# Performance work log

Hardware: AMD Instinct MI355X
Metric: run time of the kernel (lower is better)

Reference implementation:

```python
import jax, jax.numpy as jnp
import numpy as np

TOPK = 8            # args.topk
SWAP_RATIO = 0.3    # args.swap_ratio
NUM_SPECIAL = 999   # first non-special wordpiece id in bert-base-uncased


def setup_inputs() -> dict:
    key = jax.random.key(0)
    k0, k1, k2, k3, k4, k5 = jax.random.split(key, 6)
    B, S, V, D = 4, 512, 30522, 768
    return {
        "delta_grad": jax.random.normal(k0, (B, S, D), jnp.float32),
        "src_embeds": jax.random.normal(k1, (B, S, D), jnp.float32),
        "embedding_matrix": jax.random.normal(k2, (V, D), jnp.float32),
        "src_tokens": jax.random.randint(k3, (B, S), 0, V),
        "pred_lm": jax.random.normal(k4, (B, S, V), jnp.float32),
        "attention_mask": jnp.ones((B, S), jnp.int32),
        "rand_u": jax.random.uniform(k5, (B, S), jnp.float32),
    }


def reference(delta_grad, src_embeds, embedding_matrix, src_tokens, pred_lm, attention_mask, rand_u):
    B, S, D = delta_grad.shape
    V = embedding_matrix.shape[0]
    neg_inf = jnp.float32(-np.inf)

    # dir_dot_grad = -(prev_dot - new_dot) = new_dot - prev_dot
    new_dot = jnp.einsum('bsd,vd->bsv', delta_grad, embedding_matrix)   # [B,S,V]
    prev_dot = jnp.einsum('bsd,bsd->bs', delta_grad, src_embeds)        # [B,S]
    dir_dot_grad = new_dot - prev_dot[..., None]

    # pairwise euclidean distance between src_embeds and vocab embeddings
    src_sq = jnp.sum(src_embeds * src_embeds, axis=-1)                  # [B,S]
    vocab_sq = jnp.sum(embedding_matrix * embedding_matrix, axis=-1)    # [V]
    dot = jnp.einsum('bsd,vd->bsv', src_embeds, embedding_matrix)       # [B,S,V]
    sq_norm = src_sq[..., None] + vocab_sq[None, None, :] - 2.0 * dot
    dir_norm = jnp.sqrt(jax.nn.relu(sq_norm) + 1e-20)

    dir_dot_grad = dir_dot_grad / dir_norm

    # LM top-k allowed-token mask (scatter of 0 into a -inf mask in torch)
    _, topk_idx = jax.lax.top_k(pred_lm, TOPK)                          # [B,S,K]
    topk_idx = topk_idx * attention_mask[..., None].astype(topk_idx.dtype)
    bi = jnp.arange(B)[:, None, None]
    si = jnp.arange(S)[None, :, None]
    allowed = jnp.zeros((B, S, V), bool).at[bi, si, topk_idx].set(True)

    filtered = jnp.where(allowed, dir_dot_grad, neg_inf)
    # special tokens [:999] -> -inf (overrides any topk scatter there)
    filtered = jnp.where(jnp.arange(V)[None, None, :] < NUM_SPECIAL, neg_inf, filtered)
    # forbid keeping the original token
    filtered = jnp.where(jnp.arange(V)[None, None, :] == src_tokens[..., None], neg_inf, filtered)

    adv_flip = jnp.argmax(filtered, axis=2)                             # [B,S]

    # swap mask: non-special positions, Bernoulli(swap_ratio)
    no_special = src_tokens >= NUM_SPECIAL
    swap = rand_u > (1.0 - SWAP_RATIO)
    mask_idx = (no_special & swap).astype(src_tokens.dtype)

    adv_tokens = src_tokens * (1 - mask_idx) + adv_flip.astype(src_tokens.dtype) * mask_idx
    return adv_tokens
```

## Files before the change

kernel.cpp:

```cpp
#include <hip/hip_runtime.h>
#include <math.h>

constexpr int TOPK = 8;
constexpr int NUM_SPECIAL = 999;
constexpr int V = 30522;
constexpr int D = 768;
constexpr int BLOCK = 256;
constexpr int V2 = V / 2;
constexpr int NQ = 14;
constexpr int NK = (V2 + BLOCK - 1) / BLOCK;
constexpr int CAP = 512;
constexpr int HOTCAP = 64;

__device__ __forceinline__ unsigned long long fkey(float v, unsigned int idx) {
    unsigned int u = __float_as_uint(v);
    u = ((int)u < 0) ? ~u : (u | 0x80000000u);
    return ((unsigned long long)u << 32) | (unsigned long long)(~idx);
}

__device__ __forceinline__ void net8(float (&L)[TOPK], float t) {
    #pragma unroll
    for (int j = 0; j < TOPK; ++j) {
        float m = fmaxf(L[j], t); t = fminf(L[j], t); L[j] = m;
    }
}

__device__ __forceinline__ void cmpx(float& a, float& b) {
    float m = fmaxf(a, b), n = fminf(a, b); a = m; b = n;
}
__device__ __forceinline__ void bitonic_sort8_desc(float (&v)[TOPK]) {
    cmpx(v[0], v[4]); cmpx(v[1], v[5]); cmpx(v[2], v[6]); cmpx(v[3], v[7]);
    cmpx(v[0], v[2]); cmpx(v[1], v[3]); cmpx(v[4], v[6]); cmpx(v[5], v[7]);
    cmpx(v[0], v[1]); cmpx(v[2], v[3]); cmpx(v[4], v[5]); cmpx(v[6], v[7]);
}

__device__ __forceinline__ void wave_extract8(float (&cur)[TOPK], int lane,
                                              float* dst) {
    #pragma unroll
    for (int r = 0; r < TOPK; ++r) {
        float m = cur[0];
        int ml = lane;
        #pragma unroll
        for (int off = 1; off < 64; off <<= 1) {
            float om = __shfl_xor(m, off, 64);
            int   ol = __shfl_xor(ml, off, 64);
            if (om > m || (om == m && ol < ml)) { m = om; ml = ol; }
        }
        if (lane == ml) {
            #pragma unroll
            for (int j = 0; j < TOPK - 1; ++j) cur[j] = cur[j + 1];
            cur[TOPK - 1] = -INFINITY;
        }
        if (lane == 0) dst[r] = m;
    }
}

__global__ __launch_bounds__(BLOCK, 8) void dvat_kernel(
    const float* __restrict__ delta_grad,
    const float* __restrict__ src_embeds,
    const float* __restrict__ emb,
    const int*   __restrict__ src_tokens,
    const float* __restrict__ pred_lm,
    const int*   __restrict__ attn,
    const float* __restrict__ rand_u,
    int* __restrict__ out)
{
    const int pos = blockIdx.x;
    const int tid = threadIdx.x;
    const int lane = tid & 63;
    const int wave = tid >> 6;

    __shared__ float  sm32[32];
    __shared__ float  s_g8;
    __shared__ int    s_hot[HOTCAP];
    __shared__ int    s_nhot;
    __shared__ int    s_ncand;
    __shared__ unsigned long long sh_cand64[CAP];
    __shared__ int    s_cand[TOPK];
    __shared__ double s_scores[TOPK];
    __shared__ double s_pd[4], s_ssq[4];
    __shared__ float  shf[2 * D];

    if (tid == 0) { s_nhot = 0; s_ncand = 0; }

    const float2* row2 = (const float2*)(pred_lm + (size_t)pos * V);

    float vx[TOPK], vy[TOPK];
    #pragma unroll
    for (int j = 0; j < TOPK; ++j) { vx[j] = -INFINITY; vy[j] = -INFINITY; }

    int i = tid;
    for (int q = 0; q < NQ; ++q, i += 4 * BLOCK) {
        float2 a = row2[i];
        float2 b = row2[i + BLOCK];
        float2 c = row2[i + 2 * BLOCK];
        float2 d = row2[i + 3 * BLOCK];
        net8(vx, a.x); net8(vy, a.y);
        net8(vx, b.x); net8(vy, b.y);
        net8(vx, c.x); net8(vy, c.y);
        net8(vx, d.x); net8(vy, d.y);
    }
    for (; i < V2; i += BLOCK) {
        float2 f = row2[i];
        net8(vx, f.x); net8(vy, f.y);
    }

    float v8[TOPK];
    #pragma unroll
    for (int j = 0; j < TOPK; ++j) v8[j] = fmaxf(vx[j], vy[TOPK - 1 - j]);
    bitonic_sort8_desc(v8);
    const float tmax = v8[0];

    wave_extract8(v8, lane, &sm32[wave * 8]);
    __syncthreads();

    if (wave == 0) {
        float c = (lane < 32) ? sm32[lane] : -INFINITY;
        float m = -INFINITY;
        #pragma unroll
        for (int r = 0; r < TOPK; ++r) {
            m = c; int ml = lane;
            #pragma unroll
            for (int off = 1; off < 64; off <<= 1) {
                float om = __shfl_xor(m, off, 64);
                int   ol = __shfl_xor(ml, off, 64);
                if (om > m || (om == m && ol < ml)) { m = om; ml = ol; }
            }
            if (lane == ml) c = -INFINITY;
        }
        if (lane == 0) s_g8 = m;
    }
    __syncthreads();
    const float g8 = s_g8;

    if (tmax >= g8) {
        int p = atomicAdd(&s_nhot, 1);
        if (p < HOTCAP) s_hot[p] = tid;
    }
    __syncthreads();

    if (s_nhot <= HOTCAP) {
        const int nhot = s_nhot;
        const int total = nhot * NK;
        for (int w = tid; w < total; w += BLOCK) {
            const int h = w / NK;
            const int k = w - h * NK;
            const int i2 = s_hot[h] + (k << 8);
            if (i2 < V2) {
                float2 f = row2[i2];
                if (f.x >= g8) {
                    int p = atomicAdd(&s_ncand, 1);
                    if (p < CAP) sh_cand64[p] = fkey(f.x, (unsigned)(2 * i2));
                }
                if (f.y >= g8) {
                    int p = atomicAdd(&s_ncand, 1);
                    if (p < CAP) sh_cand64[p] = fkey(f.y, (unsigned)(2 * i2 + 1));
                }
            }
        }
    } else {
        for (int i2 = tid; i2 < V2; i2 += BLOCK) {
            float2 f = row2[i2];
            if (f.x >= g8) {
                int p = atomicAdd(&s_ncand, 1);
                if (p < CAP) sh_cand64[p] = fkey(f.x, (unsigned)(2 * i2));
            }
            if (f.y >= g8) {
                int p = atomicAdd(&s_ncand, 1);
                if (p < CAP) sh_cand64[p] = fkey(f.y, (unsigned)(2 * i2 + 1));
            }
        }
    }
    __syncthreads();
    const int ncand = min(s_ncand, CAP);

    for (int it = 0; it < TOPK; ++it) {
        if (tid < 64) {
            unsigned long long m = 0ull; int ms = 0;
            for (int j = tid; j < ncand; j += 64) {
                unsigned long long x = sh_cand64[j];
                if (x > m) { m = x; ms = j; }
            }
            #pragma unroll
            for (int off = 32; off; off >>= 1) {
                unsigned long long om = __shfl_down(m, off, 64);
                int os = __shfl_down(ms, off, 64);
                if (om > m) { m = om; ms = os; }
            }
            if (tid == 0) {
                s_cand[it] = (m == 0ull) ? 0 : (int)(~(unsigned int)m);
                sh_cand64[ms] = 0ull;
            }
        }
        __syncthreads();
    }

    if (tid == 0 && attn[pos] == 0) {
        #pragma unroll
        for (int k = 0; k < TOPK; ++k) s_cand[k] = 0;
    }
    __syncthreads();

    const float* dg = delta_grad + (size_t)pos * D;
    const float* se = src_embeds + (size_t)pos * D;

    double pd = 0.0, ssq = 0.0;
    for (int ii = tid; ii < D; ii += BLOCK) {
        float g = dg[ii], e = se[ii];
        shf[ii] = g;
        shf[D + ii] = e;
        pd  += (double)g * (double)e;
        ssq += (double)e * (double)e;
    }
    #pragma unroll
    for (int off = 32; off; off >>= 1) {
        pd  += __shfl_down(pd, off, 64);
        ssq += __shfl_down(ssq, off, 64);
    }
    if (lane == 0) { s_pd[wave] = pd; s_ssq[wave] = ssq; }
    __syncthreads();

    const double prev_dot = s_pd[0] + s_pd[1] + s_pd[2] + s_pd[3];
    const double src_sq   = s_ssq[0] + s_ssq[1] + s_ssq[2] + s_ssq[3];

    #pragma unroll
    for (int kk = 0; kk < 2; ++kk) {
        const int k = 2 * wave + kk;
        const int v = s_cand[k];
        const float* ev = emb + (size_t)v * D;
        double ddg = 0.0, dse = 0.0, dvv = 0.0;
        for (int ii = lane; ii < D; ii += 64) {
            double e = (double)ev[ii];
            ddg += e * (double)shf[ii];
            dse += e * (double)shf[D + ii];
            dvv += e * e;
        }
        #pragma unroll
        for (int off = 32; off; off >>= 1) {
            ddg += __shfl_down(ddg, off, 64);
            dse += __shfl_down(dse, off, 64);
            dvv += __shfl_down(dvv, off, 64);
        }
        if (lane == 0) {
            double sq = src_sq + dvv - 2.0 * dse;
            if (sq < 0.0) sq = 0.0;
            double dn = sqrt(sq + 1e-20);
            s_scores[k] = (ddg - prev_dot) / dn;
        }
    }
    __syncthreads();

    if (tid == 0) {
        const int src_tok = src_tokens[pos];
        int best = 0;
        double best_s = 0.0;
        bool found = false;
        #pragma unroll
        for (int k = 0; k < TOPK; ++k) {
            const int v = s_cand[k];
            if (v < NUM_SPECIAL || v == src_tok) continue;
            const double sc = s_scores[k];
            if (!found || sc > best_s || (sc == best_s && v < best)) {
                best = v; best_s = sc; found = true;
            }
        }
        const int adv_flip = found ? best : 0;
        const bool no_special = (src_tok >= NUM_SPECIAL);
        const bool swap = (rand_u[pos] > 0.7f);
        out[pos] = (no_special && swap) ? adv_flip : src_tok;
    }
}

extern "C" void kernel_launch(void* const* d_in, const int* in_sizes, int n_in,
                              void* d_out, int out_size, void* d_ws, size_t ws_size,
                              hipStream_t stream) {
    const float* delta_grad = (const float*)d_in[0];
    const float* src_embeds = (const float*)d_in[1];
    const float* emb        = (const float*)d_in[2];
    const int*   src_tokens = (const int*)d_in[3];
    const float* pred_lm    = (const float*)d_in[4];
    const int*   attn       = (const int*)d_in[5];
    const float* randu      = (const float*)d_in[6];
    int* out = (int*)d_out;

    const int BS = in_sizes[3];
    dvat_kernel<<<BS, BLOCK, 0, stream>>>(delta_grad, src_embeds, emb,
                                          src_tokens, pred_lm, attn, randu, out);
}
```

Baseline: 425.0 us.

## Replace per-thread top-8 network with per-thread max plus float4 row scans

The first pass over each pred_lm row now keeps only a running maximum per thread instead of an 8-wide insertion network, and derives the 8th-largest threshold from the 256 thread maxima. Rows are read as float4 with a parity-dependent 2-element offset for alignment, and the two leftover elements are checked separately by thread 0. The dot-product stage also uses float4 loads. This cuts ALU work in the memory-bound scan, but the looser threshold may admit more candidates and hot threads in the second pass.

Measured after the change: 414.5 us. 2.5% less time.

```diff
diff --git a/kernel.cpp b/kernel.cpp
--- a/kernel.cpp
+++ b/kernel.cpp
@@ -6,9 +6,8 @@
 constexpr int V = 30522;
 constexpr int D = 768;
 constexpr int BLOCK = 256;
-constexpr int V2 = V / 2;
-constexpr int NQ = 14;
-constexpr int NK = (V2 + BLOCK - 1) / BLOCK;
+constexpr int V4 = 7630;
+constexpr int NK4 = (V4 + BLOCK - 1) / BLOCK;
 constexpr int CAP = 512;
 constexpr int HOTCAP = 64;
 
@@ -23,15 +22,6 @@
     for (int j = 0; j < TOPK; ++j) {
         float m = fmaxf(L[j], t); t = fminf(L[j], t); L[j] = m;
     }
-}
-
-__device__ __forceinline__ void cmpx(float& a, float& b) {
-    float m = fmaxf(a, b), n = fminf(a, b); a = m; b = n;
-}
-__device__ __forceinline__ void bitonic_sort8_desc(float (&v)[TOPK]) {
-    cmpx(v[0], v[4]); cmpx(v[1], v[5]); cmpx(v[2], v[6]); cmpx(v[3], v[7]);
-    cmpx(v[0], v[2]); cmpx(v[1], v[3]); cmpx(v[4], v[6]); cmpx(v[5], v[7]);
-    cmpx(v[0], v[1]); cmpx(v[2], v[3]); cmpx(v[4], v[5]); cmpx(v[6], v[7]);
 }
 
 __device__ __forceinline__ void wave_extract8(float (&cur)[TOPK], int lane,
@@ -70,7 +60,8 @@
     const int lane = tid & 63;
     const int wave = tid >> 6;
 
-    __shared__ float  sm32[32];
+    __shared__ float  smax[BLOCK];
+    __shared__ float  sm8[TOPK];
     __shared__ float  s_g8;
     __shared__ int    s_hot[HOTCAP];
     __shared__ int    s_nhot;
@@ -79,96 +70,90 @@
     __shared__ int    s_cand[TOPK];
     __shared__ double s_scores[TOPK];
     __shared__ double s_pd[4], s_ssq[4];
-    __shared__ float  shf[2 * D];
+    __shared__ float4 shf4[2 * D / 4];
 
     if (tid == 0) { s_nhot = 0; s_ncand = 0; }
 
-    const float2* row2 = (const float2*)(pred_lm + (size_t)pos * V);
-
-    float vx[TOPK], vy[TOPK];
-    #pragma unroll
-    for (int j = 0; j < TOPK; ++j) { vx[j] = -INFINITY; vy[j] = -INFINITY; }
-
+    const float* rowf = pred_lm + (size_t)pos * V;
+    const int ofs = (pos & 1) << 1;
+    const float4* row4 = (const float4*)(rowf + ofs);
+
+    float m0 = -INFINITY, m1 = -INFINITY, m2 = -INFINITY, m3 = -INFINITY;
     int i = tid;
-    for (int q = 0; q < NQ; ++q, i += 4 * BLOCK) {
-        float2 a = row2[i];
-        float2 b = row2[i + BLOCK];
-        float2 c = row2[i + 2 * BLOCK];
-        float2 d = row2[i + 3 * BLOCK];
-        net8(vx, a.x); net8(vy, a.y);
-        net8(vx, b.x); net8(vy, b.y);
-        net8(vx, c.x); net8(vy, c.y);
-        net8(vx, d.x); net8(vy, d.y);
-    }
-    for (; i < V2; i += BLOCK) {
-        float2 f = row2[i];
-        net8(vx, f.x); net8(vy, f.y);
-    }
-
-    float v8[TOPK];
-    #pragma unroll
-    for (int j = 0; j < TOPK; ++j) v8[j] = fmaxf(vx[j], vy[TOPK - 1 - j]);
-    bitonic_sort8_desc(v8);
-    const float tmax = v8[0];
-
-    wave_extract8(v8, lane, &sm32[wave * 8]);
+    for (int q = 0; q < 7; ++q, i += 4 * BLOCK) {
+        float4 a = row4[i];
+        float4 b = row4[i + BLOCK];
+        float4 c = row4[i + 2 * BLOCK];
+        float4 d = row4[i + 3 * BLOCK];
+        m0 = fmaxf(m0, fmaxf(fmaxf(a.x, a.y), fmaxf(a.z, a.w)));
+        m1 = fmaxf(m1, fmaxf(fmaxf(b.x, b.y), fmaxf(b.z, b.w)));
+        m2 = fmaxf(m2, fmaxf(fmaxf(c.x, c.y), fmaxf(c.z, c.w)));
+        m3 = fmaxf(m3, fmaxf(fmaxf(d.x, d.y), fmaxf(d.z, d.w)));
+    }
+    for (; i < V4; i += BLOCK) {
+        float4 a = row4[i];
+        m0 = fmaxf(m0, fmaxf(fmaxf(a.x, a.y), fmaxf(a.z, a.w)));
+    }
+    const float tm = fmaxf(fmaxf(m0, m1), fmaxf(m2, m3));
+    smax[tid] = tm;
     __syncthreads();
 
     if (wave == 0) {
-        float c = (lane < 32) ? sm32[lane] : -INFINITY;
-        float m = -INFINITY;
-        #pragma unroll
-        for (int r = 0; r < TOPK; ++r) {
-            m = c; int ml = lane;
-            #pragma unroll
-            for (int off = 1; off < 64; off <<= 1) {
-                float om = __shfl_xor(m, off, 64);
-                int   ol = __shfl_xor(ml, off, 64);
-                if (om > m || (om == m && ol < ml)) { m = om; ml = ol; }
-            }
-            if (lane == ml) c = -INFINITY;
-        }
-        if (lane == 0) s_g8 = m;
+        float L[TOPK];
+        #pragma unroll
+        for (int j = 0; j < TOPK; ++j) L[j] = -INFINITY;
+        net8(L, smax[lane]);
+        net8(L, smax[lane + 64]);
+        net8(L, smax[lane + 128]);
+        net8(L, smax[lane + 192]);
+        wave_extract8(L, lane, sm8);
+        if (lane == 0) s_g8 = sm8[TOPK - 1];
     }
     __syncthreads();
     const float g8 = s_g8;
 
-    if (tmax >= g8) {
+    if (tm >= g8) {
         int p = atomicAdd(&s_nhot, 1);
         if (p < HOTCAP) s_hot[p] = tid;
     }
     __syncthreads();
 
+    if (tid == 0) {
+        #pragma unroll
+        for (int e = 0; e < 2; ++e) {
+            const int idx = ofs ? e : (V4 * 4 + e);
+            const float f = rowf[idx];
+            if (f >= g8) {
+                int p = atomicAdd(&s_ncand, 1);
+                if (p < CAP) sh_cand64[p] = fkey(f, (unsigned)idx);
+            }
+        }
+    }
+
     if (s_nhot <= HOTCAP) {
         const int nhot = s_nhot;
-        const int total = nhot * NK;
+        const int total = nhot * NK4;
         for (int w = tid; w < total; w += BLOCK) {
-            const int h = w / NK;
-            const int k = w - h * NK;
-            const int i2 = s_hot[h] + (k << 8);
-            if (i2 < V2) {
-                float2 f = row2[i2];
-                if (f.x >= g8) {
-                    int p = atomicAdd(&s_ncand, 1);
-                    if (p < CAP) sh_cand64[p] = fkey(f.x, (unsigned)(2 * i2));
-                }
-                if (f.y >= g8) {
-                    int p = atomicAdd(&s_ncand, 1);
-                    if (p < CAP) sh_cand64[p] = fkey(f.y, (unsigned)(2 * i2 + 1));
-                }
+            const int h = w / NK4;
+            const int k = w - h * NK4;
+            const int i4 = s_hot[h] + (k << 8);
+            if (i4 < V4) {
+                const float4 f = row4[i4];
+                const int base = ofs + 4 * i4;
+                if (f.x >= g8) { int p = atomicAdd(&s_ncand, 1); if (p < CAP) sh_cand64[p] = fkey(f.x, (unsigned)base); }
+                if (f.y >= g8) { int p = atomicAdd(&s_ncand, 1); if (p < CAP) sh_cand64[p] = fkey(f.y, (unsigned)(base + 1)); }
+                if (f.z >= g8) { int p = atomicAdd(&s_ncand, 1); if (p < CAP) sh_cand64[p] = fkey(f.z, (unsigned)(base + 2)); }
+                if (f.w >= g8) { int p = atomicAdd(&s_ncand, 1); if (p < CAP) sh_cand64[p] = fkey(f.w, (unsigned)(base + 3)); }
             }
         }
     } else {
-        for (int i2 = tid; i2 < V2; i2 += BLOCK) {
-            float2 f = row2[i2];
-            if (f.x >= g8) {
-                int p = atomicAdd(&s_ncand, 1);
-                if (p < CAP) sh_cand64[p] = fkey(f.x, (unsigned)(2 * i2));
-            }
-            if (f.y >= g8) {
-                int p = atomicAdd(&s_ncand, 1);
-                if (p < CAP) sh_cand64[p] = fkey(f.y, (unsigned)(2 * i2 + 1));
-            }
+        for (int i4 = tid; i4 < V4; i4 += BLOCK) {
+            const float4 f = row4[i4];
+            const int base = ofs + 4 * i4;
+            if (f.x >= g8) { int p = atomicAdd(&s_ncand, 1); if (p < CAP) sh_cand64[p] = fkey(f.x, (unsigned)base); }
+            if (f.y >= g8) { int p = atomicAdd(&s_ncand, 1); if (p < CAP) sh_cand64[p] = fkey(f.y, (unsigned)(base + 1)); }
+            if (f.z >= g8) { int p = atomicAdd(&s_ncand, 1); if (p < CAP) sh_cand64[p] = fkey(f.z, (unsigned)(base + 2)); }
+            if (f.w >= g8) { int p = atomicAdd(&s_ncand, 1); if (p < CAP) sh_cand64[p] = fkey(f.w, (unsigned)(base + 3)); }
         }
     }
     __syncthreads();
@@ -205,12 +190,15 @@
     const float* se = src_embeds + (size_t)pos * D;
 
     double pd = 0.0, ssq = 0.0;
-    for (int ii = tid; ii < D; ii += BLOCK) {
-        float g = dg[ii], e = se[ii];
-        shf[ii] = g;
-        shf[D + ii] = e;
-        pd  += (double)g * (double)e;
-        ssq += (double)e * (double)e;
+    for (int ii = tid; ii < D / 4; ii += BLOCK) {
+        const float4 g = ((const float4*)dg)[ii];
+        const float4 e = ((const float4*)se)[ii];
+        shf4[ii] = g;
+        shf4[D / 4 + ii] = e;
+        pd  += (double)g.x * (double)e.x + (double)g.y * (double)e.y
+             + (double)g.z * (double)e.z + (double)g.w * (double)e.w;
+        ssq += (double)e.x * (double)e.x + (double)e.y * (double)e.y
+             + (double)e.z * (double)e.z + (double)e.w * (double)e.w;
     }
     #pragma unroll
     for (int off = 32; off; off >>= 1) {
@@ -227,13 +215,18 @@
     for (int kk = 0; kk < 2; ++kk) {
         const int k = 2 * wave + kk;
         const int v = s_cand[k];
-        const float* ev = emb + (size_t)v * D;
+        const float4* ev4 = (const float4*)(emb + (size_t)v * D);
         double ddg = 0.0, dse = 0.0, dvv = 0.0;
-        for (int ii = lane; ii < D; ii += 64) {
-            double e = (double)ev[ii];
-            ddg += e * (double)shf[ii];
-            dse += e * (double)shf[D + ii];
-            dvv += e * e;
+        for (int ii = lane; ii < D / 4; ii += 64) {
+            const float4 e = ev4[ii];
+            const float4 g = shf4[ii];
+            const float4 s = shf4[D / 4 + ii];
+            ddg += (double)e.x * (double)g.x + (double)e.y * (double)g.y
+                 + (double)e.z * (double)g.z + (double)e.w * (double)g.w;
+            dse += (double)e.x * (double)s.x + (double)e.y * (double)s.y
+                 + (double)e.z * (double)s.z + (double)e.w * (double)s.w;
+            dvv += (double)e.x * (double)e.x + (double)e.y * (double)e.y
+                 + (double)e.z * (double)e.z + (double)e.w * (double)e.w;
         }
         #pragma unroll
         for (int off = 32; off; off >>= 1) {
```
